# Kernel tuning notes

Hardware: AMD Instinct MI355X
Metric: run time of the kernel (lower is better)

The kernel has to match this reference:

```python
import jax, jax.numpy as jnp
import numpy as np

B, NV, NDIRS, NRINGS, C, NF = 2, 30000, 8, 3, 16, 16


def setup_inputs() -> dict:
    key = jax.random.key(0)
    k1, k2, k3, k4, k5 = jax.random.split(key, 5)
    y = jax.random.normal(k1, (B, NV, NDIRS, C), dtype=jnp.float32)
    # sync_field: for each (batch, vertex, ring, dir) an index triple (b, v, d) into y
    v_idx = jax.random.randint(k2, (B, NV, NRINGS, NDIRS), 0, NV)
    d_idx = jax.random.randint(k3, (B, NV, NRINGS, NDIRS), 0, NDIRS)
    b_idx = jnp.broadcast_to(jnp.arange(B)[:, None, None, None], (B, NV, NRINGS, NDIRS))
    sync_field = jnp.stack([b_idx, v_idx, d_idx], axis=-1).astype(jnp.int32)
    kernel = jax.random.normal(k4, (NRINGS, NDIRS, C, NF), dtype=jnp.float32) * 0.05
    center_kernel = jax.random.normal(k5, (C, NF), dtype=jnp.float32) * 0.05
    bias = jnp.zeros((NF,), dtype=jnp.float32)
    return {"y": y, "sync_field": sync_field, "kernel": kernel,
            "center_kernel": center_kernel, "bias": bias}


def reference(y, sync_field, kernel, center_kernel, bias):
    b, nv, ndirs, c = y.shape
    nrings = kernel.shape[0]
    nf = kernel.shape[-1]
    # tf.gather_nd: index triples (batch, vertex, dir) -> channel vectors
    patches = y[sync_field[..., 0], sync_field[..., 1], sync_field[..., 2]]  # (b, nv, nrings, ndirs, c)
    patches = patches.reshape(b * nv, nrings, ndirs, c)
    # circular padding along direction axis: width becomes 2*ndirs-1
    patches = jnp.concatenate([patches, patches[:, :, :-1, :]], axis=2)
    # valid conv with (nrings, ndirs) kernel -> (b*nv, 1, ndirs, nf)
    out = jax.lax.conv_general_dilated(
        patches, kernel, window_strides=(1, 1), padding='VALID',
        dimension_numbers=('NHWC', 'HWIO', 'NHWC'))
    out = out.reshape(b, nv, ndirs, nf)
    out = out + jnp.einsum('bvdc,cf->bvdf', y, center_kernel) + bias
    out = jax.nn.relu(out)
    return jnp.max(out, axis=2)  # take_max over directions -> (b, nv, nf)
```

## Files before the change

### kernel.cpp

```cpp
#include <hip/hip_runtime.h>

static constexpr int kB = 2;
static constexpr int kNV = 30000;
static constexpr int kD = 8;
static constexpr int kR = 3;
static constexpr int kC = 16;
static constexpr int kF = 16;
static constexpr int NP = (kB * kNV) / 2;
static constexpr int S  = 3840;

typedef short short8  __attribute__((ext_vector_type(8)));
typedef float floatx4 __attribute__((ext_vector_type(4)));

static constexpr int CENT_OFS   = 1536;
static constexpr int BUF_STRIDE = 2560;

__device__ __forceinline__ unsigned bf16rne(float x) {
    unsigned u = __float_as_uint(x);
    return (u + 0x7fffu + ((u >> 16) & 1u)) >> 16;
}

__global__ __launch_bounds__(64) void sgc_kernel(
    const float* __restrict__ y,
    const int*   __restrict__ sync_field,
    const float* __restrict__ kern,
    const float* __restrict__ ck,
    const float* __restrict__ bias,
    float*       __restrict__ out)
{
    __shared__ __align__(16) char smem[2 * BUF_STRIDE];

    const int lane = threadIdx.x;
    const int wid  = blockIdx.x;
    const int f    = lane & 15;
    const int q    = lane >> 4;
    const int mvtx = (lane >> 3) & 1;
    const int md   = lane & 7;
    const int eSub = lane >> 2;
    const int iq   = lane & 3;

    {
        const int buf = lane >> 5, z = lane & 31;
        const int ofs = buf * BUF_STRIDE + CENT_OFS + (z >> 1) * 64 + 32 + (z & 1) * 16;
        *(uint4*)(smem + ofs) = make_uint4(0u, 0u, 0u, 0u);
    }

    int aOfs[12];
    short8 bfrag[13];
#pragma unroll
    for (int kk = 0; kk < 12; ++kk) {
        const int g   = kk * 4 + q;
        const int dd  = (g * 43) >> 8;
        const int rem = g - dd * 6;
        const int r   = rem >> 1;
        const int ch  = rem & 1;
        const int rot = (md + dd) & 7;
        aOfs[kk] = ((mvtx * 3 + r) * 8 + rot) * 32 + ch * 16;
        const int be = ((r * 8 + dd) * 16 + ch * 8) * 16 + f;
        union { unsigned u[4]; short8 v; } t;
#pragma unroll
        for (int j = 0; j < 4; ++j) {
            const float a = kern[be + (2 * j) * 16];
            const float b = kern[be + (2 * j + 1) * 16];
            t.u[j] = bf16rne(a) | (bf16rne(b) << 16);
        }
        bfrag[kk] = t.v;
    }
    {
        union { unsigned u[4]; short8 v; } t;
        if (q < 2) {
#pragma unroll
            for (int j = 0; j < 4; ++j) {
                const float a = ck[(q * 8 + 2 * j) * 16 + f];
                const float b = ck[(q * 8 + 2 * j + 1) * 16 + f];
                t.u[j] = bf16rne(a) | (bf16rne(b) << 16);
            }
        } else {
            t.u[0] = t.u[1] = t.u[2] = t.u[3] = 0u;
        }
        bfrag[12] = t.v;
    }
    const float biasv = bias[f];

    auto cl = [](int v) { return v < NP ? v : NP - 1; };

    int tA[3], tB[3], tC[3];
    float4 A0, A1, A2, Ac, B0, B1, B2, Bc;

#define SF_PRE(cc) do { \
        const int base_ = (cc) * 48; \
        _Pragma("unroll") \
        for (int g_ = 0; g_ < 3; ++g_) { \
            const int* s_ = sync_field + (size_t)(base_ + g_ * 16 + eSub) * 3; \
            tA[g_] = s_[0]; tB[g_] = s_[1]; tC[g_] = s_[2]; \
        } \
    } while (0)

#define ISSUE_G(Rv, cc) do { \
        { const float4* gp_ = reinterpret_cast<const float4*>( \
              y + ((tA[0] * kNV + tB[0]) * kD + tC[0]) * kC) + iq; Rv##0 = *gp_; } \
        { const float4* gp_ = reinterpret_cast<const float4*>( \
              y + ((tA[1] * kNV + tB[1]) * kD + tC[1]) * kC) + iq; Rv##1 = *gp_; } \
        { const float4* gp_ = reinterpret_cast<const float4*>( \
              y + ((tA[2] * kNV + tB[2]) * kD + tC[2]) * kC) + iq; Rv##2 = *gp_; } \
        Rv##c = reinterpret_cast<const float4*>(y + (size_t)(cc) * 256)[lane]; \
    } while (0)

#define STAGE(Rv, bufbase) do { \
        const float4 gg_[3] = { Rv##0, Rv##1, Rv##2 }; \
        _Pragma("unroll") \
        for (int g_ = 0; g_ < 3; ++g_) { \
            uint2 w_; \
            w_.x = bf16rne(gg_[g_].x) | (bf16rne(gg_[g_].y) << 16); \
            w_.y = bf16rne(gg_[g_].z) | (bf16rne(gg_[g_].w) << 16); \
            *(uint2*)((bufbase) + g_ * 512 + lane * 8) = w_; \
        } \
        { \
            uint2 w_; \
            w_.x = bf16rne(Rv##c.x) | (bf16rne(Rv##c.y) << 16); \
            w_.y = bf16rne(Rv##c.z) | (bf16rne(Rv##c.w) << 16); \
            *(uint2*)((bufbase) + CENT_OFS + eSub * 64 + iq * 8) = w_; \
        } \
    } while (0)

#define DRAIN do { \
        __asm__ __volatile__("" ::: "memory"); \
        __builtin_amdgcn_s_waitcnt(0xC07F);  \
        __asm__ __volatile__("" ::: "memory"); \
    } while (0)

#define COMPUTE_STORE(bufbase, pp) do { \
        floatx4 acc0 = { biasv, biasv, biasv, biasv }; \
        floatx4 acc1 = { 0.f, 0.f, 0.f, 0.f }; \
        _Pragma("unroll") \
        for (int kk_ = 0; kk_ < 12; kk_ += 2) { \
            const short8 a0_ = *(const short8*)((bufbase) + aOfs[kk_]); \
            const short8 a1_ = *(const short8*)((bufbase) + aOfs[kk_ + 1]); \
            acc0 = __builtin_amdgcn_mfma_f32_16x16x32_bf16(a0_, bfrag[kk_], acc0, 0, 0, 0); \
            acc1 = __builtin_amdgcn_mfma_f32_16x16x32_bf16(a1_, bfrag[kk_ + 1], acc1, 0, 0, 0); \
        } \
        { \
            const short8 ac_ = *(const short8*)((bufbase) + CENT_OFS \
                                                + (lane & 15) * 64 + q * 16); \
            acc0 = __builtin_amdgcn_mfma_f32_16x16x32_bf16(ac_, bfrag[12], acc0, 0, 0, 0); \
        } \
        float mx = fmaxf(fmaxf(acc0[0] + acc1[0], acc0[1] + acc1[1]), \
                         fmaxf(acc0[2] + acc1[2], acc0[3] + acc1[3])); \
        mx = fmaxf(mx, 0.0f); \
        mx = fmaxf(mx, __shfl_xor(mx, 16, 64)); \
        if (((lane >> 4) & 1) == 0) \
            out[(2 * (pp) + (lane >> 5)) * kF + f] = mx; \
    } while (0)

    int p = wid;
    SF_PRE(p);
    ISSUE_G(A, p);
    SF_PRE(cl(p + S));
    ISSUE_G(B, cl(p + S));
    SF_PRE(cl(p + 2 * S));
    STAGE(A, smem);
    ISSUE_G(A, cl(p + 2 * S));
    SF_PRE(cl(p + 3 * S));

    for (;;) {
        STAGE(B, smem + BUF_STRIDE);
        ISSUE_G(B, cl(p + 3 * S));
        SF_PRE(cl(p + 4 * S));
        DRAIN;
        COMPUTE_STORE(smem, p);
        p += S; if (p >= NP) break;

        STAGE(A, smem);
        ISSUE_G(A, cl(p + 3 * S));
        SF_PRE(cl(p + 4 * S));
        DRAIN;
        COMPUTE_STORE(smem + BUF_STRIDE, p);
        p += S; if (p >= NP) break;
    }

#undef SF_PRE
#undef ISSUE_G
#undef STAGE
#undef DRAIN
#undef COMPUTE_STORE
}

extern "C" void kernel_launch(void* const* d_in, const int* in_sizes, int n_in,
                              void* d_out, int out_size, void* d_ws, size_t ws_size,
                              hipStream_t stream) {
    const float* y    = reinterpret_cast<const float*>(d_in[0]);
    const int*   sf   = reinterpret_cast<const int*>(d_in[1]);
    const float* kern = reinterpret_cast<const float*>(d_in[2]);
    const float* ck   = reinterpret_cast<const float*>(d_in[3]);
    const float* bias = reinterpret_cast<const float*>(d_in[4]);
    float* out = reinterpret_cast<float*>(d_out);

    sgc_kernel<<<S, 64, 0, stream>>>(y, sf, kern, ck, bias, out);
}
```

Before: 113.2 us.

## Use packed bf16 conversion intrinsic, precompute gather offsets, retune grid and occupancy

Replaces the manual integer round-to-nearest-even bf16 conversion with the HIP __float22bfloat162_rn intrinsic, which may lower to a hardware packed conversion instruction. Sync-field triples are folded into a single byte offset at prefetch time instead of being kept as three registers and multiplied out at issue time. Grid stride S rises from 3840 to 4096 and launch bounds add a minimum-blocks hint of 4. This trims ALU work and register pressure in the staging loop, at the cost of a different tail balance across blocks.

```diff
diff --git a/kernel.cpp b/kernel.cpp
--- a/kernel.cpp
+++ b/kernel.cpp
@@ -1,4 +1,5 @@
 #include <hip/hip_runtime.h>
+#include <hip/hip_bf16.h>
 
 static constexpr int kB = 2;
 static constexpr int kNV = 30000;
@@ -7,7 +8,7 @@
 static constexpr int kC = 16;
 static constexpr int kF = 16;
 static constexpr int NP = (kB * kNV) / 2;
-static constexpr int S  = 3840;
+static constexpr int S  = 4096;
 
 typedef short short8  __attribute__((ext_vector_type(8)));
 typedef float floatx4 __attribute__((ext_vector_type(4)));
@@ -15,12 +16,13 @@
 static constexpr int CENT_OFS   = 1536;
 static constexpr int BUF_STRIDE = 2560;
 
-__device__ __forceinline__ unsigned bf16rne(float x) {
-    unsigned u = __float_as_uint(x);
-    return (u + 0x7fffu + ((u >> 16) & 1u)) >> 16;
+__device__ __forceinline__ unsigned pkbf16(float lo, float hi) {
+    union { __hip_bfloat162 h; unsigned u; } cv;
+    cv.h = __float22bfloat162_rn(make_float2(lo, hi));
+    return cv.u;
 }
 
-__global__ __launch_bounds__(64) void sgc_kernel(
+__global__ __launch_bounds__(64, 4) void sgc_kernel(
     const float* __restrict__ y,
     const int*   __restrict__ sync_field,
     const float* __restrict__ kern,
@@ -59,22 +61,17 @@
         const int be = ((r * 8 + dd) * 16 + ch * 8) * 16 + f;
         union { unsigned u[4]; short8 v; } t;
 #pragma unroll
-        for (int j = 0; j < 4; ++j) {
-            const float a = kern[be + (2 * j) * 16];
-            const float b = kern[be + (2 * j + 1) * 16];
-            t.u[j] = bf16rne(a) | (bf16rne(b) << 16);
-        }
+        for (int j = 0; j < 4; ++j)
+            t.u[j] = pkbf16(kern[be + (2 * j) * 16], kern[be + (2 * j + 1) * 16]);
         bfrag[kk] = t.v;
     }
     {
         union { unsigned u[4]; short8 v; } t;
         if (q < 2) {
 #pragma unroll
-            for (int j = 0; j < 4; ++j) {
-                const float a = ck[(q * 8 + 2 * j) * 16 + f];
-                const float b = ck[(q * 8 + 2 * j + 1) * 16 + f];
-                t.u[j] = bf16rne(a) | (bf16rne(b) << 16);
-            }
+            for (int j = 0; j < 4; ++j)
+                t.u[j] = pkbf16(ck[(q * 8 + 2 * j) * 16 + f],
+                                ck[(q * 8 + 2 * j + 1) * 16 + f]);
         } else {
             t.u[0] = t.u[1] = t.u[2] = t.u[3] = 0u;
         }
@@ -84,7 +81,7 @@
 
     auto cl = [](int v) { return v < NP ? v : NP - 1; };
 
-    int tA[3], tB[3], tC[3];
+    int off[3];
     float4 A0, A1, A2, Ac, B0, B1, B2, Bc;
 
 #define SF_PRE(cc) do { \
@@ -92,35 +89,31 @@
         _Pragma("unroll") \
         for (int g_ = 0; g_ < 3; ++g_) { \
             const int* s_ = sync_field + (size_t)(base_ + g_ * 16 + eSub) * 3; \
-            tA[g_] = s_[0]; tB[g_] = s_[1]; tC[g_] = s_[2]; \
+            off[g_] = ((s_[0] * kNV + s_[1]) * kD + s_[2]) * 64 + iq * 16; \
         } \
     } while (0)
 
 #define ISSUE_G(Rv, cc) do { \
-        { const float4* gp_ = reinterpret_cast<const float4*>( \
-              y + ((tA[0] * kNV + tB[0]) * kD + tC[0]) * kC) + iq; Rv##0 = *gp_; } \
-        { const float4* gp_ = reinterpret_cast<const float4*>( \
-              y + ((tA[1] * kNV + tB[1]) * kD + tC[1]) * kC) + iq; Rv##1 = *gp_; } \
-        { const float4* gp_ = reinterpret_cast<const float4*>( \
-              y + ((tA[2] * kNV + tB[2]) * kD + tC[2]) * kC) + iq; Rv##2 = *gp_; } \
+        Rv##0 = *reinterpret_cast<const float4*>( \
+                    reinterpret_cast<const char*>(y) + off[0]); \
+        Rv##1 = *reinterpret_cast<const float4*>( \
+                    reinterpret_cast<const char*>(y) + off[1]); \
+        Rv##2 = *reinterpret_cast<const float4*>( \
+                    reinterpret_cast<const char*>(y) + off[2]); \
         Rv##c = reinterpret_cast<const float4*>(y + (size_t)(cc) * 256)[lane]; \
     } while (0)
 
 #define STAGE(Rv, bufbase) do { \
-        const float4 gg_[3] = { Rv##0, Rv##1, Rv##2 }; \
-        _Pragma("unroll") \
-        for (int g_ = 0; g_ < 3; ++g_) { \
-            uint2 w_; \
-            w_.x = bf16rne(gg_[g_].x) | (bf16rne(gg_[g_].y) << 16); \
-            w_.y = bf16rne(gg_[g_].z) | (bf16rne(gg_[g_].w) << 16); \
-            *(uint2*)((bufbase) + g_ * 512 + lane * 8) = w_; \
-        } \
-        { \
-            uint2 w_; \
-            w_.x = bf16rne(Rv##c.x) | (bf16rne(Rv##c.y) << 16); \
-            w_.y = bf16rne(Rv##c.z) | (bf16rne(Rv##c.w) << 16); \
-            *(uint2*)((bufbase) + CENT_OFS + eSub * 64 + iq * 8) = w_; \
-        } \
+        const float4 g0_ = Rv##0, g1_ = Rv##1, g2_ = Rv##2, gc_ = Rv##c; \
+        uint2 w_; \
+        w_.x = pkbf16(g0_.x, g0_.y); w_.y = pkbf16(g0_.z, g0_.w); \
+        *(uint2*)((bufbase) + 0 * 512 + lane * 8) = w_; \
+        w_.x = pkbf16(g1_.x, g1_.y); w_.y = pkbf16(g1_.z, g1_.w); \
+        *(uint2*)((bufbase) + 1 * 512 + lane * 8) = w_; \
+        w_.x = pkbf16(g2_.x, g2_.y); w_.y = pkbf16(g2_.z, g2_.w); \
+        *(uint2*)((bufbase) + 2 * 512 + lane * 8) = w_; \
+        w_.x = pkbf16(gc_.x, gc_.y); w_.y = pkbf16(gc_.z, gc_.w); \
+        *(uint2*)((bufbase) + CENT_OFS + eSub * 64 + iq * 8) = w_; \
     } while (0)
 
 #define DRAIN do { \
```

New measurement: 131.2 us. 15.9% more time.
